# Performance work log

Hardware: AMD Instinct MI355X
Metric: run time of the kernel (lower is better)

Reference implementation:

```python
import jax, jax.numpy as jnp
import numpy as np

EPS_NORM = 1e-12   # F.normalize eps (denominator clamp)
EPS_PD = 1e-6      # F.pairwise_distance eps (added to the difference)
MARGIN = 0.3

B, D = 8192, 512


def setup_inputs() -> dict:
    key = jax.random.key(0)
    x = jax.random.normal(key, (B, D * 2), dtype=jnp.float32).reshape(B, 2, D)
    return {"x": x}


def reference(x):
    # x: [B, 2, D]  (anchor, positive)
    a = x[:, 0, :]
    p = x[:, 1, :]
    a = a / jnp.maximum(jnp.linalg.norm(a, axis=1, keepdims=True), EPS_NORM)
    p = p / jnp.maximum(jnp.linalg.norm(p, axis=1, keepdims=True), EPS_NORM)
    b, d = a.shape

    # output[i, j] = -||a_i - p_j + EPS_PD||^2, expanded so the BxB matrix
    # comes from one GEMM instead of a [B, D, B] broadcasted difference.
    sa2 = jnp.sum(a * a, axis=1)               # [B]
    sp2 = jnp.sum(p * p, axis=1)               # [B]
    dot = a @ p.T                              # [B, B]
    sa = jnp.sum(a, axis=1)                    # [B]
    sp = jnp.sum(p, axis=1)                    # [B]
    d2 = (sa2[:, None] + sp2[None, :] - 2.0 * dot
          + 2.0 * EPS_PD * (sa[:, None] - sp[None, :]) + d * (EPS_PD * EPS_PD))
    sim = -d2                                  # [B, B] similarity (detached in torch)

    # mineHardNegative with hard_rank=0, hard_prob=1: top-1 of descending sort
    # after removing the self index -> argmax over the row with diag masked.
    sim = jnp.where(jnp.eye(b, dtype=bool), -jnp.inf, sim)
    negidx = jnp.argmax(sim, axis=1)           # [B] int
    n = p[negidx]                              # hard negatives, [B, D]

    pos_d = jnp.linalg.norm(a - p + EPS_PD, axis=1)
    neg_d = jnp.linalg.norm(a - n + EPS_PD, axis=1)
    nloss = jnp.mean(jax.nn.relu(pos_d ** 2 - neg_d ** 2 + MARGIN))
    return nloss
```

## Files before the change

kernel.cpp:

```cpp
#include <hip/hip_runtime.h>
#include <stdint.h>
#include <math.h>

#define Bn 8192
#define Dn 512
#define EPSN 1e-12f
#define EPSP 1e-6f
#define MARG 0.3f

#define BM 128
#define BN 128
#define BKB 64
#define KT (Dn / BKB)
#define NCT (Bn / BN)
#define QS 256.0f
#define ISQ (2.0f / 65536.0f)

typedef int   int4v __attribute__((ext_vector_type(4)));
typedef float f32x4 __attribute__((ext_vector_type(4)));

__device__ __forceinline__ void async16(const void* g, void* l) {
    __builtin_amdgcn_global_load_lds(
        (const __attribute__((address_space(1))) void*)g,
        (__attribute__((address_space(3))) void*)l,
        16, 0, 0);
}

__device__ __forceinline__ unsigned key32(float s) {
    union { float f; unsigned u; } c; c.f = s;
    return (c.u & 0x80000000u) ? ~c.u : (c.u | 0x80000000u);
}
__device__ __forceinline__ float unkey32(unsigned k) {
    union { unsigned u; float f; } c;
    c.u = (k & 0x80000000u) ? (k ^ 0x80000000u) : ~k;
    return c.f;
}

__global__ __launch_bounds__(256) void k_normalize(
    const float* __restrict__ x,
    uint8_t* __restrict__ a_i8, uint8_t* __restrict__ p_i8,
    float* __restrict__ cterm, float* __restrict__ rowconst,
    unsigned* __restrict__ rowmax)
{
    const int wave = threadIdx.x >> 6;
    const int lane = threadIdx.x & 63;
    const int i = blockIdx.x * 4 + wave;

    const float* srcA = x + (size_t)i * (2 * Dn) + lane * 8;
    const float* srcP = srcA + Dn;
    float4 a0 = ((const float4*)srcA)[0];
    float4 a1 = ((const float4*)srcA)[1];
    float4 p0 = ((const float4*)srcP)[0];
    float4 p1 = ((const float4*)srcP)[1];
    float va[8] = {a0.x, a0.y, a0.z, a0.w, a1.x, a1.y, a1.z, a1.w};
    float vp[8] = {p0.x, p0.y, p0.z, p0.w, p1.x, p1.y, p1.z, p1.w};

    float ssa = 0.f, ssp = 0.f;
#pragma unroll
    for (int j = 0; j < 8; ++j) { ssa += va[j] * va[j]; ssp += vp[j] * vp[j]; }
#pragma unroll
    for (int m = 1; m < 64; m <<= 1) {
        ssa += __shfl_xor(ssa, m);
        ssp += __shfl_xor(ssp, m);
    }
    const float sa = 1.0f / fmaxf(sqrtf(ssa), EPSN);
    const float sp = 1.0f / fmaxf(sqrtf(ssp), EPSN);

    float oa[8], op[8];
    float s1p = 0.f, s2p = 0.f, s1a = 0.f, s2a = 0.f, pos = 0.f;
#pragma unroll
    for (int j = 0; j < 8; ++j) {
        oa[j] = va[j] * sa;
        op[j] = vp[j] * sp;
        s1p += op[j]; s2p += op[j] * op[j];
        s1a += oa[j]; s2a += oa[j] * oa[j];
        const float u = oa[j] - op[j] + EPSP;
        pos += u * u;
    }

    uint64_t pka = 0, pkp = 0;
#pragma unroll
    for (int j = 0; j < 8; ++j) {
        int qa = (int)rintf(oa[j] * QS);
        int qp = (int)rintf(op[j] * QS);
        qa = qa > 127 ? 127 : (qa < -127 ? -127 : qa);
        qp = qp > 127 ? 127 : (qp < -127 ? -127 : qp);
        pka |= (uint64_t)(uint8_t)qa << (8 * j);
        pkp |= (uint64_t)(uint8_t)qp << (8 * j);
    }
    *(uint64_t*)(a_i8 + (size_t)i * Dn + lane * 8) = pka;
    *(uint64_t*)(p_i8 + (size_t)i * Dn + lane * 8) = pkp;

#pragma unroll
    for (int m = 1; m < 64; m <<= 1) {
        s1p += __shfl_xor(s1p, m);
        s2p += __shfl_xor(s2p, m);
        s1a += __shfl_xor(s1a, m);
        s2a += __shfl_xor(s2a, m);
        pos += __shfl_xor(pos, m);
    }
    if (lane == 0) {
        cterm[i] = -s2p + 2.0f * EPSP * s1p;
        rowconst[i] = pos - s2a - 2.0f * EPSP * s1a
                      - (float)Dn * EPSP * EPSP + MARG;
        rowmax[i] = 0u;
    }
}

__global__ __launch_bounds__(256, 4) void k_gemm_argmax(
    const uint8_t* __restrict__ a_i8, const uint8_t* __restrict__ p_i8,
    const float* __restrict__ cterm,
    unsigned* __restrict__ rowmax)
{
    __shared__ uint8_t As[2][BM * BKB];
    __shared__ uint8_t Bs[2][BN * BKB];
    __shared__ unsigned sm[2][BN];

    const int t = threadIdx.x;
    const int wave = t >> 6;
    const int lane = t & 63;
    const int rowBase = blockIdx.y * BM;
    const int colBase = blockIdx.x * BN;

    const int q = lane >> 4;
    const int m16 = lane & 15;
    const int waveRow = (wave >> 1) * 64;
    const int waveCol = (wave & 1) * 64;

    const int r0 = t >> 2;
    const int g0 = (t & 3) ^ ((r0 >> 1) & 3);
    const int r1 = (256 + t) >> 2;
    const int g1 = ((256 + t) & 3) ^ ((r1 >> 1) & 3);
    const uint8_t* gA0 = p_i8 + (size_t)(rowBase + r0) * Dn + g0 * 16;
    const uint8_t* gA1 = p_i8 + (size_t)(rowBase + r1) * Dn + g1 * 16;
    const uint8_t* gB0 = a_i8 + (size_t)(colBase + r0) * Dn + g0 * 16;
    const uint8_t* gB1 = a_i8 + (size_t)(colBase + r1) * Dn + g1 * 16;
    const int ldsC0 = (wave * 64) * 16;
    const int ldsC1 = (256 + wave * 64) * 16;

    const int s0 = q ^ ((m16 >> 1) & 3);
    const int aBase = (waveRow + m16) * BKB + s0 * 16;
    const int bBase = (waveCol + m16) * BKB + s0 * 16;

    int4v acc[4][4];
#pragma unroll
    for (int a = 0; a < 4; ++a)
#pragma unroll
        for (int b = 0; b < 4; ++b) acc[a][b] = (int4v){0, 0, 0, 0};

    auto stage = [&](int buf, int ke) {
        async16(gA0 + ke, &As[buf][ldsC0]);
        async16(gA1 + ke, &As[buf][ldsC1]);
        async16(gB0 + ke, &Bs[buf][ldsC0]);
        async16(gB1 + ke, &Bs[buf][ldsC1]);
    };

    stage(0, 0);
#pragma unroll
    for (int kt = 0; kt < KT; ++kt) {
        const int cur = kt & 1;
        __syncthreads();
        if (kt + 1 < KT) stage(cur ^ 1, (kt + 1) * BKB);

        const uint8_t* pa = &As[cur][aBase];
        const uint8_t* pb = &Bs[cur][bBase];
        int4v af[4], bfr[4];
#pragma unroll
        for (int mt = 0; mt < 4; ++mt)
            af[mt] = *(const int4v*)(pa + mt * 16 * BKB);
#pragma unroll
        for (int nt = 0; nt < 4; ++nt)
            bfr[nt] = *(const int4v*)(pb + nt * 16 * BKB);
#pragma unroll
        for (int mt = 0; mt < 4; ++mt)
#pragma unroll
            for (int nt = 0; nt < 4; ++nt)
                acc[mt][nt] = __builtin_amdgcn_mfma_i32_16x16x64_i8(
                    af[mt], bfr[nt], acc[mt][nt], 0, 0, 0);
    }

    f32x4 cj[4];
#pragma unroll
    for (int mt = 0; mt < 4; ++mt)
        cj[mt] = *(const f32x4*)(cterm + rowBase + waveRow + mt * 16 + q * 4);

    unsigned kv[4];
    const bool diag = (rowBase == colBase);
    if (!diag) {
#pragma unroll
        for (int nt = 0; nt < 4; ++nt) {
            float mx = -3.4e38f;
#pragma unroll
            for (int mt = 0; mt < 4; ++mt)
#pragma unroll
                for (int v = 0; v < 4; ++v)
                    mx = fmaxf(mx, ISQ * (float)acc[mt][nt][v] + cj[mt][v]);
            kv[nt] = key32(mx);
        }
    } else {
#pragma unroll
        for (int nt = 0; nt < 4; ++nt) {
            const int dtarget = waveCol - waveRow + nt * 16 + m16 - q * 4;
            float mx = -3.4e38f;
#pragma unroll
            for (int mt = 0; mt < 4; ++mt)
#pragma unroll
                for (int v = 0; v < 4; ++v) {
                    const float sc = ISQ * (float)acc[mt][nt][v] + cj[mt][v];
                    mx = (mt * 16 + v == dtarget) ? mx : fmaxf(mx, sc);
                }
            kv[nt] = key32(mx);
        }
    }

#pragma unroll
    for (int nt = 0; nt < 4; ++nt) {
#pragma unroll
        for (int msk = 16; msk < 64; msk <<= 1) {
            const unsigned o = (unsigned)__shfl_xor((int)kv[nt], msk);
            kv[nt] = o > kv[nt] ? o : kv[nt];
        }
    }
    if (lane < 16) {
#pragma unroll
        for (int nt = 0; nt < 4; ++nt)
            sm[wave >> 1][(wave & 1) * 64 + nt * 16 + m16] = kv[nt];
    }
    __syncthreads();
    if (t < BN) {
        const unsigned k0 = sm[0][t];
        const unsigned k1 = sm[1][t];
        atomicMax(&rowmax[colBase + t], k0 > k1 ? k0 : k1);
    }
}

__global__ __launch_bounds__(1024) void k_final(
    const unsigned* __restrict__ rowmax,
    const float* __restrict__ rowconst,
    float* __restrict__ out)
{
    __shared__ float smf[16];
    float s = 0.f;
    for (int k = threadIdx.x; k < Bn; k += 1024)
        s += fmaxf(rowconst[k] + unkey32(rowmax[k]), 0.f);
#pragma unroll
    for (int msk = 1; msk < 64; msk <<= 1) s += __shfl_xor(s, msk);
    if ((threadIdx.x & 63) == 0) smf[threadIdx.x >> 6] = s;
    __syncthreads();
    if (threadIdx.x == 0) {
        float tot = 0.f;
#pragma unroll
        for (int w = 0; w < 16; ++w) tot += smf[w];
        out[0] = tot * (1.0f / Bn);
    }
}

extern "C" void kernel_launch(void* const* d_in, const int* in_sizes, int n_in,
                              void* d_out, int out_size, void* d_ws, size_t ws_size,
                              hipStream_t stream)
{
    const float* x = (const float*)d_in[0];
    char* ws = (char*)d_ws;
    uint8_t*  a_i8     = (uint8_t*)(ws + 0);
    uint8_t*  p_i8     = (uint8_t*)(ws + 4194304);
    float*    cterm    = (float*)(ws + 8388608);
    float*    rowconst = (float*)(ws + 8421376);
    unsigned* rowmax   = (unsigned*)(ws + 8454144);
    float*    out      = (float*)d_out;

    k_normalize<<<2048, 256, 0, stream>>>(x, a_i8, p_i8, cterm, rowconst, rowmax);
    k_gemm_argmax<<<dim3(NCT, Bn / BM), 256, 0, stream>>>(a_i8, p_i8, cterm, rowmax);
    k_final<<<1, 1024, 0, stream>>>(rowmax, rowconst, out);
}
```

Baseline: 117.7 us.

## Enlarge GEMM tile to 256x256 with 4-slot LDS ring and interleaved staging

```diff
diff --git a/kernel.cpp b/kernel.cpp
--- a/kernel.cpp
+++ b/kernel.cpp
@@ -7,14 +7,12 @@
 #define EPSN 1e-12f
 #define EPSP 1e-6f
 #define MARG 0.3f
-
-#define BM 128
-#define BN 128
-#define BKB 64
-#define KT (Dn / BKB)
-#define NCT (Bn / BN)
 #define QS 256.0f
 #define ISQ (2.0f / 65536.0f)
+
+
+#define TKB 64
+#define NKT (Dn / TKB)
 
 typedef int   int4v __attribute__((ext_vector_type(4)));
 typedef float f32x4 __attribute__((ext_vector_type(4)));
@@ -107,91 +105,112 @@
     }
 }
 
-__global__ __launch_bounds__(256, 4) void k_gemm_argmax(
+__global__ __launch_bounds__(512, 2) void k_gemm_argmax(
     const uint8_t* __restrict__ a_i8, const uint8_t* __restrict__ p_i8,
     const float* __restrict__ cterm,
     unsigned* __restrict__ rowmax)
 {
-    __shared__ uint8_t As[2][BM * BKB];
-    __shared__ uint8_t Bs[2][BN * BKB];
-    __shared__ unsigned sm[2][BN];
+    __shared__ __align__(16) uint8_t As[4][256 * TKB];
+    __shared__ __align__(16) uint8_t Bs[4][256 * TKB];
+    __shared__ unsigned smx[2][256];
 
     const int t = threadIdx.x;
     const int wave = t >> 6;
     const int lane = t & 63;
-    const int rowBase = blockIdx.y * BM;
-    const int colBase = blockIdx.x * BN;
-
     const int q = lane >> 4;
     const int m16 = lane & 15;
-    const int waveRow = (wave >> 1) * 64;
-    const int waveCol = (wave & 1) * 64;
-
-    const int r0 = t >> 2;
-    const int g0 = (t & 3) ^ ((r0 >> 1) & 3);
-    const int r1 = (256 + t) >> 2;
-    const int g1 = ((256 + t) & 3) ^ ((r1 >> 1) & 3);
-    const uint8_t* gA0 = p_i8 + (size_t)(rowBase + r0) * Dn + g0 * 16;
-    const uint8_t* gA1 = p_i8 + (size_t)(rowBase + r1) * Dn + g1 * 16;
-    const uint8_t* gB0 = a_i8 + (size_t)(colBase + r0) * Dn + g0 * 16;
-    const uint8_t* gB1 = a_i8 + (size_t)(colBase + r1) * Dn + g1 * 16;
-    const int ldsC0 = (wave * 64) * 16;
-    const int ldsC1 = (256 + wave * 64) * 16;
-
-    const int s0 = q ^ ((m16 >> 1) & 3);
-    const int aBase = (waveRow + m16) * BKB + s0 * 16;
-    const int bBase = (waveCol + m16) * BKB + s0 * 16;
-
-    int4v acc[4][4];
-#pragma unroll
-    for (int a = 0; a < 4; ++a)
+    const int wr = wave >> 2;
+    const int wc = wave & 3;
+    const int j0 = blockIdx.y * 256;
+    const int i0 = blockIdx.x * 256;
+
+    const int rr = t >> 2;
+    const int gg = ((t & 3) ^ ((t >> 3) & 3)) * 16;
+    const uint8_t* gA0 = p_i8 + (size_t)(j0 + rr) * Dn + gg;
+    const uint8_t* gA1 = p_i8 + (size_t)(j0 + 128 + rr) * Dn + gg;
+    const uint8_t* gB0 = a_i8 + (size_t)(i0 + rr) * Dn + gg;
+    const uint8_t* gB1 = a_i8 + (size_t)(i0 + 128 + rr) * Dn + gg;
+    const int ldsOff = wave * 1024;
+
+    const int sl = (q ^ ((m16 >> 1) & 3)) * 16;
+    const int aOff = (wr * 128 + m16) * TKB + sl;
+    const int bOff = (wc * 64 + m16) * TKB + sl;
+
+    auto stage1 = [&](int slot, int kb, int h) {
+        switch (h) {
+        case 0: async16(gA0 + kb, &As[slot][ldsOff]);        break;
+        case 1: async16(gA1 + kb, &As[slot][8192 + ldsOff]); break;
+        case 2: async16(gB0 + kb, &Bs[slot][ldsOff]);        break;
+        case 3: async16(gB1 + kb, &Bs[slot][8192 + ldsOff]); break;
+        }
+    };
+
+    int4v acc[8][4];
+#pragma unroll
+    for (int a = 0; a < 8; ++a)
 #pragma unroll
         for (int b = 0; b < 4; ++b) acc[a][b] = (int4v){0, 0, 0, 0};
 
-    auto stage = [&](int buf, int ke) {
-        async16(gA0 + ke, &As[buf][ldsC0]);
-        async16(gA1 + ke, &As[buf][ldsC1]);
-        async16(gB0 + ke, &Bs[buf][ldsC0]);
-        async16(gB1 + ke, &Bs[buf][ldsC1]);
-    };
-
-    stage(0, 0);
-#pragma unroll
-    for (int kt = 0; kt < KT; ++kt) {
-        const int cur = kt & 1;
-        __syncthreads();
-        if (kt + 1 < KT) stage(cur ^ 1, (kt + 1) * BKB);
-
-        const uint8_t* pa = &As[cur][aBase];
-        const uint8_t* pb = &Bs[cur][bBase];
-        int4v af[4], bfr[4];
-#pragma unroll
-        for (int mt = 0; mt < 4; ++mt)
-            af[mt] = *(const int4v*)(pa + mt * 16 * BKB);
-#pragma unroll
-        for (int nt = 0; nt < 4; ++nt)
-            bfr[nt] = *(const int4v*)(pb + nt * 16 * BKB);
-#pragma unroll
-        for (int mt = 0; mt < 4; ++mt)
+#pragma unroll
+    for (int h = 0; h < 4; ++h) stage1(0, 0, h);
+#pragma unroll
+    for (int h = 0; h < 4; ++h) stage1(1, TKB, h);
+    asm volatile("s_waitcnt vmcnt(4)" ::: "memory");
+    __builtin_amdgcn_s_barrier();
+
+#pragma unroll
+    for (int kt = 0; kt < NKT; ++kt) {
+        const int slot = kt & 3;
+        const uint8_t* pa = &As[slot][aOff];
+        const uint8_t* pb = &Bs[slot][bOff];
+        int4v bf[4];
+#pragma unroll
+        for (int p = 0; p < 4; ++p) {
+            int4v af0 = *(const int4v*)(pa + (2 * p) * 1024);
+            int4v af1 = *(const int4v*)(pa + (2 * p + 1) * 1024);
+            if (p == 0) {
+#pragma unroll
+                for (int nt = 0; nt < 4; ++nt)
+                    bf[nt] = *(const int4v*)(pb + nt * 1024);
+            }
+            if (kt + 2 < NKT) stage1((kt + 2) & 3, (kt + 2) * TKB, p);
+
+            __builtin_amdgcn_s_barrier();
+            asm volatile("s_waitcnt lgkmcnt(0)" ::: "memory");
+            __builtin_amdgcn_sched_barrier(0);
+            __builtin_amdgcn_s_setprio(1);
 #pragma unroll
             for (int nt = 0; nt < 4; ++nt)
-                acc[mt][nt] = __builtin_amdgcn_mfma_i32_16x16x64_i8(
-                    af[mt], bfr[nt], acc[mt][nt], 0, 0, 0);
-    }
-
-    f32x4 cj[4];
-#pragma unroll
-    for (int mt = 0; mt < 4; ++mt)
-        cj[mt] = *(const f32x4*)(cterm + rowBase + waveRow + mt * 16 + q * 4);
+                acc[2 * p][nt] = __builtin_amdgcn_mfma_i32_16x16x64_i8(
+                    af0, bf[nt], acc[2 * p][nt], 0, 0, 0);
+#pragma unroll
+            for (int nt = 0; nt < 4; ++nt)
+                acc[2 * p + 1][nt] = __builtin_amdgcn_mfma_i32_16x16x64_i8(
+                    af1, bf[nt], acc[2 * p + 1][nt], 0, 0, 0);
+            __builtin_amdgcn_s_setprio(0);
+            if (p == 3) {
+                if (kt + 2 < NKT)
+                    asm volatile("s_waitcnt vmcnt(4)" ::: "memory");
+                else if (kt + 2 == NKT)
+                    asm volatile("s_waitcnt vmcnt(0)" ::: "memory");
+            }
+            __builtin_amdgcn_s_barrier();
+        }
+    }
+
+    f32x4 cj[8];
+#pragma unroll
+    for (int mt = 0; mt < 8; ++mt)
+        cj[mt] = *(const f32x4*)(cterm + j0 + wr * 128 + mt * 16 + q * 4);
 
     unsigned kv[4];
-    const bool diag = (rowBase == colBase);
+    const bool diag = (i0 == j0);
     if (!diag) {
 #pragma unroll
         for (int nt = 0; nt < 4; ++nt) {
             float mx = -3.4e38f;
 #pragma unroll
-            for (int mt = 0; mt < 4; ++mt)
+            for (int mt = 0; mt < 8; ++mt)
 #pragma unroll
                 for (int v = 0; v < 4; ++v)
                     mx = fmaxf(mx, ISQ * (float)acc[mt][nt][v] + cj[mt][v]);
@@ -200,10 +219,10 @@
     } else {
 #pragma unroll
         for (int nt = 0; nt < 4; ++nt) {
-            const int dtarget = waveCol - waveRow + nt * 16 + m16 - q * 4;
+            const int dtarget = wc * 64 + nt * 16 + m16 - wr * 128 - q * 4;
             float mx = -3.4e38f;
 #pragma unroll
-            for (int mt = 0; mt < 4; ++mt)
+            for (int mt = 0; mt < 8; ++mt)
 #pragma unroll
                 for (int v = 0; v < 4; ++v) {
                     const float sc = ISQ * (float)acc[mt][nt][v] + cj[mt][v];
@@ -224,13 +243,13 @@
     if (lane < 16) {
 #pragma unroll
         for (int nt = 0; nt < 4; ++nt)
-            sm[wave >> 1][(wave & 1) * 64 + nt * 16 + m16] = kv[nt];
+            smx[wr][wc * 64 + nt * 16 + m16] = kv[nt];
     }
     __syncthreads();
-    if (t < BN) {
-        const unsigned k0 = sm[0][t];
-        const unsigned k1 = sm[1][t];
-        atomicMax(&rowmax[colBase + t], k0 > k1 ? k0 : k1);
+    if (t < 256) {
+        const unsigned k0 = smx[0][t];
+        const unsigned k1 = smx[1][t];
+        atomicMax(&rowmax[i0 + t], k0 > k1 ? k0 : k1);
     }
 }
 
@@ -269,6 +288,7 @@
     float*    out      = (float*)d_out;
 
     k_normalize<<<2048, 256, 0, stream>>>(x, a_i8, p_i8, cterm, rowconst, rowmax);
-    k_gemm_argmax<<<dim3(NCT, Bn / BM), 256, 0, stream>>>(a_i8, p_i8, cterm, rowmax);
+    k_gemm_argmax<<<dim3(Bn / 256, Bn / 256), 512, 0, stream>>>(
+        a_i8, p_i8, cterm, rowmax);
     k_final<<<1, 1024, 0, stream>>>(rowmax, rowconst, out);
 }
```

After: 119.3 us. About the same (+1.3%).
